# Kernel optimization log

Measured on AMD Instinct MI355X. Metric: run time of the kernel, lower is better.

Reference implementation:

```python
import jax, jax.numpy as jnp
import numpy as np

DIM, HEADS, WS, SHIFT = 192, 6, 8, 4
HEAD_DIM = DIM // HEADS
SCALE = HEAD_DIM ** -0.5
EPS = 1e-5


def _rel_pos_index(ws):
    coords = np.stack(np.meshgrid(np.arange(ws), np.arange(ws), indexing='ij'))  # [2,ws,ws]
    flat = coords.reshape(2, -1)
    rel = flat[:, :, None] - flat[:, None, :]          # [2,N,N]
    rel = rel.transpose(1, 2, 0)
    rel[:, :, 0] += ws - 1
    rel[:, :, 1] += ws - 1
    rel[:, :, 0] *= 2 * ws - 1
    return rel.sum(-1)                                  # [N,N] int


def _attn_mask(H, W, ws, shift):
    if shift == 0:
        return None
    img = np.zeros((H, W), dtype=np.float32)
    cnt = 0
    for hs in (slice(0, -ws), slice(-ws, -shift), slice(-shift, None)):
        for wsl in (slice(0, -ws), slice(-ws, -shift), slice(-shift, None)):
            img[hs, wsl] = cnt
            cnt += 1
    mw = img.reshape(H // ws, ws, W // ws, ws).transpose(0, 2, 1, 3).reshape(-1, ws * ws)  # [nW,N]
    m = mw[:, None, :] - mw[:, :, None]
    return jnp.asarray(np.where(m != 0, -100.0, 0.0).astype(np.float32))  # [nW,N,N]


def _ln(x, w, b):
    mu = x.mean(-1, keepdims=True)
    var = ((x - mu) ** 2).mean(-1, keepdims=True)
    return (x - mu) * jax.lax.rsqrt(var + EPS) * w + b


def setup_inputs() -> dict:
    key = jax.random.key(0)
    ks = jax.random.split(key, 10)
    B, H, W, C = 64, 56, 56, DIM
    hid = 4 * C
    p = lambda k, sh, s=0.02: jax.random.normal(k, sh, jnp.float32) * s
    return {
        'x': jax.random.normal(ks[0], (B, H * W, C), jnp.float32),
        'ln1_w': jnp.ones((C,), jnp.float32), 'ln1_b': jnp.zeros((C,), jnp.float32),
        'qkv_w': p(ks[1], (C, 3 * C)), 'qkv_b': jnp.zeros((3 * C,), jnp.float32),
        'proj_w': p(ks[2], (C, C)), 'proj_b': jnp.zeros((C,), jnp.float32),
        'rpb_table': p(ks[3], ((2 * WS - 1) ** 2, HEADS)),
        'ln2_w': jnp.ones((C,), jnp.float32), 'ln2_b': jnp.zeros((C,), jnp.float32),
        'fc1_w': p(ks[4], (C, hid)), 'fc1_b': jnp.zeros((hid,), jnp.float32),
        'fc2_w': p(ks[5], (hid, C)), 'fc2_b': jnp.zeros((C,), jnp.float32),
        'H': H, 'W': W,
    }


def reference(x, ln1_w, ln1_b, qkv_w, qkv_b, proj_w, proj_b, rpb_table,
              ln2_w, ln2_b, fc1_w, fc1_b, fc2_w, fc2_b, H, W):
    B, L, C = x.shape
    N = WS * WS
    shortcut = x
    xn = _ln(x, ln1_w, ln1_b).reshape(B, H, W, C)
    xn = jnp.roll(xn, (-SHIFT, -SHIFT), (1, 2))
    # window partition -> [B*nW, N, C]
    xw = xn.reshape(B, H // WS, WS, W // WS, WS, C).transpose(0, 1, 3, 2, 4, 5)
    xw = xw.reshape(-1, N, C)
    B_ = xw.shape[0]
    qkv = (xw @ qkv_w + qkv_b).reshape(B_, N, 3, HEADS, HEAD_DIM).transpose(2, 0, 3, 1, 4)
    q, k, v = qkv[0], qkv[1], qkv[2]                    # [B_,h,N,d]
    attn = jnp.einsum('bhnd,bhmd->bhnm', q * SCALE, k)
    bias = rpb_table[_rel_pos_index(WS).reshape(-1)].reshape(N, N, HEADS).transpose(2, 0, 1)
    attn = attn + bias[None]
    mask = _attn_mask(H, W, WS, SHIFT)
    if mask is not None:
        nW = mask.shape[0]
        attn = attn.reshape(B_ // nW, nW, HEADS, N, N) + mask[None, :, None]
        attn = attn.reshape(B_, HEADS, N, N)
    attn = jax.nn.softmax(attn, axis=-1)
    out = jnp.einsum('bhnm,bhmd->bhnd', attn, v).transpose(0, 2, 1, 3).reshape(B_, N, C)
    out = out @ proj_w + proj_b
    # window reverse
    out = out.reshape(B, H // WS, W // WS, WS, WS, C).transpose(0, 1, 3, 2, 4, 5).reshape(B, H, W, C)
    out = jnp.roll(out, (SHIFT, SHIFT), (1, 2))
    x = shortcut + out.reshape(B, L, C)
    h = jax.nn.gelu(_ln(x, ln2_w, ln2_b) @ fc1_w + fc1_b, approximate=False)
    return x + (h @ fc2_w + fc2_b)
```

## Files before the change

### kernel.cpp

```cpp
#include <hip/hip_runtime.h>
#include <cstdint>
#include <cstddef>

#define WS_ 8
#define DIM_ 192
#define HEADS_ 6
#define HD_ 32
#define HH_ 56
#define NW_ 7
#define NWIN_ 49
#define LTOK_ 3136
#define NTOK_ 200704
#define NWTOT_ 3136
#define SHIFT_ 4
#define SCALE_ 0.17677669529663687f

typedef unsigned short ushort_t;
typedef __attribute__((ext_vector_type(8))) short short8;
typedef __attribute__((ext_vector_type(4))) float floatx4;
typedef __attribute__((ext_vector_type(8))) unsigned short ushort8;

__device__ __forceinline__ float b2f(ushort_t u) {
    union { unsigned int i; float f; } c; c.i = ((unsigned int)u) << 16; return c.f;
}
__device__ __forceinline__ ushort_t f2b(float f) {
    union { float f; unsigned int i; } c; c.f = f;
    unsigned int u = c.i;
    unsigned int r = (u + 0x7FFFu + ((u >> 16) & 1u)) >> 16;
    return (ushort_t)r;
}

__device__ __forceinline__ void load_lds16(const void* g, void* l) {
    __builtin_amdgcn_global_load_lds(
        (const __attribute__((address_space(1))) unsigned int*)g,
        (__attribute__((address_space(3))) unsigned int*)l, 16, 0, 0);
}

__device__ __forceinline__ int win_row_to_img(int r) {
    int win = r >> 6, n = r & 63;
    int b = win / NWIN_, wI = win - b * NWIN_;
    int wh = wI / NW_, wwi = wI - wh * NW_;
    int i = n >> 3, j = n & 7;
    int hh = wh * WS_ + i + SHIFT_; if (hh >= HH_) hh -= HH_;
    int ww = wwi * WS_ + j + SHIFT_; if (ww >= HH_) ww -= HH_;
    return b * LTOK_ + hh * HH_ + ww;
}

__global__ void transpose_kernel(const float* __restrict__ in,
                                 ushort_t* __restrict__ out, int K, int N) {
    int id = blockIdx.x * 256 + threadIdx.x;
    if (id >= K * N) return;
    int k = id / N, n = id - k * N;
    out[(size_t)n * K + k] = f2b(in[id]);
}

template <bool PERMUTE>
__global__ __launch_bounds__(256) void ln_kernel(const float* __restrict__ xin,
                                                 const float* __restrict__ w,
                                                 const float* __restrict__ bia,
                                                 ushort_t* __restrict__ out,
                                                 int rowOff) {
    int t = blockIdx.x * 4 + (threadIdx.x >> 6);
    int lane = threadIdx.x & 63;
    int src = PERMUTE ? win_row_to_img(rowOff + t) : t;
    const float* xp = xin + (size_t)src * DIM_;
    float v0 = xp[lane];
    float v1 = xp[lane + 64];
    float v2 = xp[lane + 128];
    float s = v0 + v1 + v2;
    float ss = v0 * v0 + v1 * v1 + v2 * v2;
#pragma unroll
    for (int o = 32; o > 0; o >>= 1) {
        s += __shfl_xor(s, o);
        ss += __shfl_xor(ss, o);
    }
    float mu = s * (1.0f / 192.0f);
    float var = ss * (1.0f / 192.0f) - mu * mu;
    float inv = rsqrtf(var + 1e-5f);
    ushort_t* op = out + (size_t)t * DIM_;
    op[lane]       = f2b((v0 - mu) * inv * w[lane]       + bia[lane]);
    op[lane + 64]  = f2b((v1 - mu) * inv * w[lane + 64]  + bia[lane + 64]);
    op[lane + 128] = f2b((v2 - mu) * inv * w[lane + 128] + bia[lane + 128]);
}

#define EPI_STORE 0
#define EPI_GELU 1
#define EPI_PROJ 2
#define EPI_FC2 3

template <int EPI>
__global__ __launch_bounds__(256) void gemm_kernel(const ushort_t* __restrict__ A,
                                                   const ushort_t* __restrict__ Bt,
                                                   const float* __restrict__ bias,
                                                   void* __restrict__ outv,
                                                   const float* __restrict__ aux,
                                                   int K, int N, int rowOff) {
    __shared__ char smem[40960];

    int tid = threadIdx.x;
    int wave = tid >> 6, lane = tid & 63;
    int quad = lane >> 4, l16 = lane & 15;
    int wave_r = wave >> 1, wave_c = wave & 1;
    int row0 = blockIdx.x * 128;
    int n0 = blockIdx.y * 192;

    floatx4 acc[4][6];
#pragma unroll
    for (int rt = 0; rt < 4; ++rt)
#pragma unroll
        for (int ct = 0; ct < 6; ++ct)
#pragma unroll
            for (int e = 0; e < 4; ++e) acc[rt][ct][e] = 0.0f;

    int nk = K >> 5;

    auto stage = [&](int kk, int buf) {
#pragma unroll
        for (int j = 0; j < 2; ++j) {
            int o = (tid + j * 256) * 16;
            int row = o >> 6, kb = o & 63;
            const ushort_t* g = A + (size_t)(row0 + row) * K + kk * 32 + (kb >> 1);
            load_lds16(g, smem + buf * 8192 + o);
        }
#pragma unroll
        for (int j = 0; j < 3; ++j) {
            int o = (tid + j * 256) * 16;
            int row = o >> 6, kb = o & 63;
            const ushort_t* g = Bt + (size_t)(n0 + row) * K + kk * 32 + (kb >> 1);
            load_lds16(g, smem + 16384 + buf * 12288 + o);
        }
    };

    stage(0, 0);
    for (int kk = 0; kk < nk; ++kk) {
        int cur = kk & 1;
        __syncthreads();
        if (kk + 1 < nk) stage(kk + 1, cur ^ 1);

        short8 a[4];
#pragma unroll
        for (int rt = 0; rt < 4; ++rt)
            a[rt] = *(const short8*)(smem + cur * 8192 +
                     ((wave_r * 64 + rt * 16 + l16) * 64 + quad * 16));
#pragma unroll
        for (int ct = 0; ct < 6; ++ct) {
            short8 b = *(const short8*)(smem + 16384 + cur * 12288 +
                        ((wave_c * 96 + ct * 16 + l16) * 64 + quad * 16));
#pragma unroll
            for (int rt = 0; rt < 4; ++rt)
                acc[rt][ct] = __builtin_amdgcn_mfma_f32_16x16x32_bf16(a[rt], b, acc[rt][ct], 0, 0, 0);
        }
    }

#pragma unroll
    for (int ct = 0; ct < 6; ++ct) {
        int c = n0 + wave_c * 96 + ct * 16 + l16;
        float bs = bias[c];
#pragma unroll
        for (int rt = 0; rt < 4; ++rt) {
#pragma unroll
            for (int r = 0; r < 4; ++r) {
                int rr = row0 + wave_r * 64 + rt * 16 + quad * 4 + r;
                float val = acc[rt][ct][r] + bs;
                if (EPI == EPI_STORE) {
                    ((ushort_t*)outv)[(size_t)rr * N + c] = f2b(val);
                } else if (EPI == EPI_GELU) {
                    float g = 0.5f * val * (1.0f + erff(val * 0.70710678118654752f));
                    ((ushort_t*)outv)[(size_t)rr * N + c] = f2b(g);
                } else if (EPI == EPI_PROJ) {
                    int dst = win_row_to_img(rowOff + rr);
                    size_t idx = (size_t)dst * DIM_ + c;
                    ((float*)outv)[idx] = val + aux[idx];
                } else {
                    size_t idx = (size_t)rr * DIM_ + c;
                    ((float*)outv)[idx] = val + aux[idx];
                }
            }
        }
    }
}

__global__ __launch_bounds__(256) void attn_kernel(const ushort_t* __restrict__ qkv,
                                                   const float* __restrict__ rpb,
                                                   ushort_t* __restrict__ aout,
                                                   int win0) {
    __shared__ float qs[64][36], ks[64][36], vs[64][36];
    __shared__ float S[64][65];
    __shared__ int regid[64];
    int bid = blockIdx.x;
    int winl = bid / HEADS_, head = bid - winl * HEADS_;
    int wI = (win0 + winl) % NWIN_;
    int wh = wI / NW_, wwi = wI - wh * NW_;
    int tid = threadIdx.x;
    int row = tid >> 2, c0 = (tid & 3) * 8;
    size_t base = (size_t)(winl * 64 + row) * (3 * DIM_) + head * HD_ + c0;
    ushort8 qv = *(const ushort8*)(qkv + base);
    ushort8 kv = *(const ushort8*)(qkv + base + DIM_);
    ushort8 vv = *(const ushort8*)(qkv + base + 2 * DIM_);
#pragma unroll
    for (int e = 0; e < 8; ++e) {
        qs[row][c0 + e] = b2f(qv[e]) * SCALE_;
        ks[row][c0 + e] = b2f(kv[e]);
        vs[row][c0 + e] = b2f(vv[e]);
    }
    if (tid < 64) {
        int i = tid >> 3, j = tid & 7;
        int hh = wh * WS_ + i, ww = wwi * WS_ + j;
        int rh = (hh < HH_ - WS_) ? 0 : ((hh < HH_ - SHIFT_) ? 1 : 2);
        int rw = (ww < HH_ - WS_) ? 0 : ((ww < HH_ - SHIFT_) ? 1 : 2);
        regid[tid] = rh * 3 + rw;
    }
    __syncthreads();

    int n = tid >> 2, qq = tid & 3;
    float qr[32];
#pragma unroll
    for (int e = 0; e < 8; ++e) {
        floatx4 t4 = *(const floatx4*)&qs[n][e * 4];
        qr[e * 4 + 0] = t4[0]; qr[e * 4 + 1] = t4[1];
        qr[e * 4 + 2] = t4[2]; qr[e * 4 + 3] = t4[3];
    }
    int i1 = n >> 3, j1 = n & 7;
    int rg1 = regid[n];
#pragma unroll 4
    for (int mi = 0; mi < 16; ++mi) {
        int m = mi * 4 + qq;
        float d = 0.0f;
#pragma unroll
        for (int e = 0; e < 8; ++e) {
            floatx4 k4 = *(const floatx4*)&ks[m][e * 4];
            d += qr[e * 4 + 0] * k4[0] + qr[e * 4 + 1] * k4[1] +
                 qr[e * 4 + 2] * k4[2] + qr[e * 4 + 3] * k4[3];
        }
        int i2 = m >> 3, j2 = m & 7;
        int rel = (i1 - i2 + 7) * 15 + (j1 - j2 + 7);
        d += rpb[rel * HEADS_ + head];
        if (regid[m] != rg1) d -= 100.0f;
        S[n][m] = d;
    }
    __syncthreads();

    if (tid < 64) {
        float mx = -1e30f;
        for (int m = 0; m < 64; ++m) mx = fmaxf(mx, S[tid][m]);
        float sum = 0.0f;
        for (int m = 0; m < 64; ++m) {
            float e = __expf(S[tid][m] - mx);
            S[tid][m] = e;
            sum += e;
        }
        float rs = 1.0f / sum;
        for (int m = 0; m < 64; ++m) S[tid][m] *= rs;
    }
    __syncthreads();

    int d0 = (tid & 3) * 8;
    float o[8];
#pragma unroll
    for (int e = 0; e < 8; ++e) o[e] = 0.0f;
    for (int m = 0; m < 64; ++m) {
        float p = S[n][m];
        floatx4 va = *(const floatx4*)&vs[m][d0];
        floatx4 vb = *(const floatx4*)&vs[m][d0 + 4];
        o[0] += p * va[0]; o[1] += p * va[1]; o[2] += p * va[2]; o[3] += p * va[3];
        o[4] += p * vb[0]; o[5] += p * vb[1]; o[6] += p * vb[2]; o[7] += p * vb[3];
    }
    ushort8 pk;
#pragma unroll
    for (int e = 0; e < 8; ++e) pk[e] = f2b(o[e]);
    *(ushort8*)(aout + (size_t)(winl * 64 + n) * DIM_ + head * HD_ + d0) = pk;
}

extern "C" void kernel_launch(void* const* d_in, const int* in_sizes, int n_in,
                              void* d_out, int out_size, void* d_ws, size_t ws_size,
                              hipStream_t stream) {
    const float* x      = (const float*)d_in[0];
    const float* ln1_w  = (const float*)d_in[1];
    const float* ln1_b  = (const float*)d_in[2];
    const float* qkv_w  = (const float*)d_in[3];
    const float* qkv_b  = (const float*)d_in[4];
    const float* proj_w = (const float*)d_in[5];
    const float* proj_b = (const float*)d_in[6];
    const float* rpb    = (const float*)d_in[7];
    const float* ln2_w  = (const float*)d_in[8];
    const float* ln2_b  = (const float*)d_in[9];
    const float* fc1_w  = (const float*)d_in[10];
    const float* fc1_b  = (const float*)d_in[11];
    const float* fc2_w  = (const float*)d_in[12];
    const float* fc2_b  = (const float*)d_in[13];

    char* ws = (char*)d_ws;
    size_t off = 0;
    auto alloc = [&](size_t bytes) -> void* {
        void* p = ws + off;
        off += (bytes + 255) & ~(size_t)255;
        return p;
    };
    ushort_t* qkv_wt  = (ushort_t*)alloc((size_t)576 * 192 * 2);
    ushort_t* proj_wt = (ushort_t*)alloc((size_t)192 * 192 * 2);
    ushort_t* fc1_wt  = (ushort_t*)alloc((size_t)768 * 192 * 2);
    ushort_t* fc2_wt  = (ushort_t*)alloc((size_t)192 * 768 * 2);

    float* x1 = (float*)d_out;

    size_t budget = (ws_size > off + 4096) ? (ws_size - off - 4096) : 0;
    long rows = (long)(budget / 1920);
    rows = (rows / 128) * 128;
    if (rows < 128) rows = 128;
    if (rows > NTOK_) rows = NTOK_;
    int chunkRows = (int)rows;
    int Wc = chunkRows / 64;
    if (Wc > NWTOT_) Wc = NWTOT_;

    ushort_t* bufS = (ushort_t*)alloc((size_t)chunkRows * 192 * 2);
    ushort_t* bufL = (ushort_t*)alloc((size_t)chunkRows * 768 * 2);
    (void)n_in; (void)in_sizes; (void)out_size;

    transpose_kernel<<<(192 * 576 + 255) / 256, 256, 0, stream>>>(qkv_w, qkv_wt, 192, 576);
    transpose_kernel<<<(192 * 192 + 255) / 256, 256, 0, stream>>>(proj_w, proj_wt, 192, 192);
    transpose_kernel<<<(192 * 768 + 255) / 256, 256, 0, stream>>>(fc1_w, fc1_wt, 192, 768);
    transpose_kernel<<<(768 * 192 + 255) / 256, 256, 0, stream>>>(fc2_w, fc2_wt, 768, 192);

    for (int w0 = 0; w0 < NWTOT_; w0 += Wc) {
        int wc = NWTOT_ - w0 < Wc ? NWTOT_ - w0 : Wc;
        int rowsA = wc * 64;
        ln_kernel<true><<<rowsA / 4, 256, 0, stream>>>(x, ln1_w, ln1_b, bufS, w0 * 64);
        dim3 gq(rowsA / 128, 576 / 192);
        gemm_kernel<EPI_STORE><<<gq, 256, 0, stream>>>(bufS, qkv_wt, qkv_b, bufL, nullptr, 192, 576, 0);
        attn_kernel<<<wc * HEADS_, 256, 0, stream>>>(bufL, rpb, bufS, w0);
        dim3 gp(rowsA / 128, 1);
        gemm_kernel<EPI_PROJ><<<gp, 256, 0, stream>>>(bufS, proj_wt, proj_b, x1, x, 192, 192, w0 * 64);
    }

    for (int t0 = 0; t0 < NTOK_; t0 += chunkRows) {
        int tc = NTOK_ - t0 < chunkRows ? NTOK_ - t0 : chunkRows;
        ln_kernel<false><<<tc / 4, 256, 0, stream>>>(x1 + (size_t)t0 * 192, ln2_w, ln2_b, bufS, 0);
        dim3 g1(tc / 128, 768 / 192);
        gemm_kernel<EPI_GELU><<<g1, 256, 0, stream>>>(bufS, fc1_wt, fc1_b, bufL, nullptr, 192, 768, 0);
        dim3 g2(tc / 128, 1);
        gemm_kernel<EPI_FC2><<<g2, 256, 0, stream>>>(bufL, fc2_wt, fc2_b,
                                                     x1 + (size_t)t0 * 192,
                                                     x1 + (size_t)t0 * 192, 768, 192, 0);
    }
}
```

Before: 1.243 ms.

## Rewrite window attention with MFMA, one wave per window-head, and precomputed bias+mask

```diff
diff --git a/kernel.cpp b/kernel.cpp
--- a/kernel.cpp
+++ b/kernel.cpp
@@ -17,6 +17,7 @@
 
 typedef unsigned short ushort_t;
 typedef __attribute__((ext_vector_type(8))) short short8;
+typedef __attribute__((ext_vector_type(4))) short bf16x4;
 typedef __attribute__((ext_vector_type(4))) float floatx4;
 typedef __attribute__((ext_vector_type(8))) unsigned short ushort8;
 
@@ -52,6 +53,23 @@
     if (id >= K * N) return;
     int k = id / N, n = id - k * N;
     out[(size_t)n * K + k] = f2b(in[id]);
+}
+
+__global__ void bias_kernel(const float* __restrict__ rpb, float* __restrict__ Spre) {
+    int th = blockIdx.x;
+    int type = th / HEADS_, head = th - type * HEADS_;
+    for (int idx = threadIdx.x; idx < 4096; idx += 256) {
+        int q = idx >> 6, k = idx & 63;
+        int i1 = q >> 3, j1 = q & 7, i2 = k >> 3, j2 = k & 7;
+        int rel = (i1 - i2 + 7) * 15 + (j1 - j2 + 7);
+        float v = rpb[rel * HEADS_ + head];
+        int rh1 = (type & 2) ? (i1 < 4 ? 1 : 2) : 0;
+        int rw1 = (type & 1) ? (j1 < 4 ? 1 : 2) : 0;
+        int rh2 = (type & 2) ? (i2 < 4 ? 1 : 2) : 0;
+        int rw2 = (type & 1) ? (j2 < 4 ? 1 : 2) : 0;
+        if (rh1 != rh2 || rw1 != rw2) v -= 100.0f;
+        Spre[(size_t)th * 4096 + idx] = v;
+    }
 }
 
 template <bool PERMUTE>
@@ -87,6 +105,7 @@
 #define EPI_GELU 1
 #define EPI_PROJ 2
 #define EPI_FC2 3
+#define EPI_QKV 4
 
 template <int EPI>
 __global__ __launch_bounds__(256) void gemm_kernel(const ushort_t* __restrict__ A,
@@ -164,6 +183,9 @@
                 float val = acc[rt][ct][r] + bs;
                 if (EPI == EPI_STORE) {
                     ((ushort_t*)outv)[(size_t)rr * N + c] = f2b(val);
+                } else if (EPI == EPI_QKV) {
+                    float sv = (c < DIM_) ? val * SCALE_ : val;
+                    ((ushort_t*)outv)[(size_t)rr * N + c] = f2b(sv);
                 } else if (EPI == EPI_GELU) {
                     float g = 0.5f * val * (1.0f + erff(val * 0.70710678118654752f));
                     ((ushort_t*)outv)[(size_t)rr * N + c] = f2b(g);
@@ -181,94 +203,119 @@
 }
 
 __global__ __launch_bounds__(256) void attn_kernel(const ushort_t* __restrict__ qkv,
-                                                   const float* __restrict__ rpb,
+                                                   const float* __restrict__ Spre,
                                                    ushort_t* __restrict__ aout,
-                                                   int win0) {
-    __shared__ float qs[64][36], ks[64][36], vs[64][36];
-    __shared__ float S[64][65];
-    __shared__ int regid[64];
-    int bid = blockIdx.x;
-    int winl = bid / HEADS_, head = bid - winl * HEADS_;
+                                                   int win0, int nwh) {
+    __shared__ char smem[32768];
+    int wave = threadIdx.x >> 6;
+    int whid = blockIdx.x * 4 + wave;
+    if (whid >= nwh) return;
+    int lane = threadIdx.x & 63;
+    int l16 = lane & 15, quad = lane >> 4;
+    int winl = whid / HEADS_, head = whid - winl * HEADS_;
     int wI = (win0 + winl) % NWIN_;
     int wh = wI / NW_, wwi = wI - wh * NW_;
-    int tid = threadIdx.x;
-    int row = tid >> 2, c0 = (tid & 3) * 8;
-    size_t base = (size_t)(winl * 64 + row) * (3 * DIM_) + head * HD_ + c0;
-    ushort8 qv = *(const ushort8*)(qkv + base);
-    ushort8 kv = *(const ushort8*)(qkv + base + DIM_);
-    ushort8 vv = *(const ushort8*)(qkv + base + 2 * DIM_);
-#pragma unroll
-    for (int e = 0; e < 8; ++e) {
-        qs[row][c0 + e] = b2f(qv[e]) * SCALE_;
-        ks[row][c0 + e] = b2f(kv[e]);
-        vs[row][c0 + e] = b2f(vv[e]);
-    }
-    if (tid < 64) {
-        int i = tid >> 3, j = tid & 7;
-        int hh = wh * WS_ + i, ww = wwi * WS_ + j;
-        int rh = (hh < HH_ - WS_) ? 0 : ((hh < HH_ - SHIFT_) ? 1 : 2);
-        int rw = (ww < HH_ - WS_) ? 0 : ((ww < HH_ - SHIFT_) ? 1 : 2);
-        regid[tid] = rh * 3 + rw;
-    }
-    __syncthreads();
-
-    int n = tid >> 2, qq = tid & 3;
-    float qr[32];
-#pragma unroll
-    for (int e = 0; e < 8; ++e) {
-        floatx4 t4 = *(const floatx4*)&qs[n][e * 4];
-        qr[e * 4 + 0] = t4[0]; qr[e * 4 + 1] = t4[1];
-        qr[e * 4 + 2] = t4[2]; qr[e * 4 + 3] = t4[3];
-    }
-    int i1 = n >> 3, j1 = n & 7;
-    int rg1 = regid[n];
-#pragma unroll 4
-    for (int mi = 0; mi < 16; ++mi) {
-        int m = mi * 4 + qq;
-        float d = 0.0f;
-#pragma unroll
-        for (int e = 0; e < 8; ++e) {
-            floatx4 k4 = *(const floatx4*)&ks[m][e * 4];
-            d += qr[e * 4 + 0] * k4[0] + qr[e * 4 + 1] * k4[1] +
-                 qr[e * 4 + 2] * k4[2] + qr[e * 4 + 3] * k4[3];
-        }
-        int i2 = m >> 3, j2 = m & 7;
-        int rel = (i1 - i2 + 7) * 15 + (j1 - j2 + 7);
-        d += rpb[rel * HEADS_ + head];
-        if (regid[m] != rg1) d -= 100.0f;
-        S[n][m] = d;
-    }
-    __syncthreads();
-
-    if (tid < 64) {
-        float mx = -1e30f;
-        for (int m = 0; m < 64; ++m) mx = fmaxf(mx, S[tid][m]);
-        float sum = 0.0f;
-        for (int m = 0; m < 64; ++m) {
-            float e = __expf(S[tid][m] - mx);
-            S[tid][m] = e;
-            sum += e;
-        }
-        float rs = 1.0f / sum;
-        for (int m = 0; m < 64; ++m) S[tid][m] *= rs;
-    }
-    __syncthreads();
-
-    int d0 = (tid & 3) * 8;
-    float o[8];
-#pragma unroll
-    for (int e = 0; e < 8; ++e) o[e] = 0.0f;
-    for (int m = 0; m < 64; ++m) {
-        float p = S[n][m];
-        floatx4 va = *(const floatx4*)&vs[m][d0];
-        floatx4 vb = *(const floatx4*)&vs[m][d0 + 4];
-        o[0] += p * va[0]; o[1] += p * va[1]; o[2] += p * va[2]; o[3] += p * va[3];
-        o[4] += p * vb[0]; o[5] += p * vb[1]; o[6] += p * vb[2]; o[7] += p * vb[3];
-    }
-    ushort8 pk;
-#pragma unroll
-    for (int e = 0; e < 8; ++e) pk[e] = f2b(o[e]);
-    *(ushort8*)(aout + (size_t)(winl * 64 + n) * DIM_ + head * HD_ + d0) = pk;
+    int type = ((wh == 6) ? 2 : 0) + ((wwi == 6) ? 1 : 0);
+
+    const ushort_t* qb = qkv + (size_t)(winl * 64) * 576 + head * HD_;
+
+    short8 vfrag[2][2];
+#pragma unroll
+    for (int kk = 0; kk < 2; ++kk)
+#pragma unroll
+        for (int dt = 0; dt < 2; ++dt)
+#pragma unroll
+            for (int e = 0; e < 8; ++e)
+                vfrag[dt][kk][e] =
+                    (short)qb[(size_t)(kk * 32 + quad * 8 + e) * 576 + 2 * DIM_ + dt * 16 + l16];
+
+    short8 kf[4], qf[4];
+#pragma unroll
+    for (int t = 0; t < 4; ++t) {
+        kf[t] = *(const short8*)(qb + (size_t)(t * 16 + l16) * 576 + DIM_ + quad * 8);
+        qf[t] = *(const short8*)(qb + (size_t)(t * 16 + l16) * 576 + quad * 8);
+    }
+
+    const float* bp = Spre + (size_t)(type * HEADS_ + head) * 4096;
+    floatx4 acc[4][4];
+#pragma unroll
+    for (int art = 0; art < 4; ++art)
+#pragma unroll
+        for (int act = 0; act < 4; ++act)
+            acc[art][act] = *(const floatx4*)(bp + (act * 16 + l16) * 64 + art * 16 + quad * 4);
+
+#pragma unroll
+    for (int art = 0; art < 4; ++art)
+#pragma unroll
+        for (int act = 0; act < 4; ++act)
+            acc[art][act] = __builtin_amdgcn_mfma_f32_16x16x32_bf16(
+                kf[art], qf[act], acc[art][act], 0, 0, 0);
+
+    char* pb = smem + wave * 8192;
+    int sw = (l16 & 7) << 4;
+#pragma unroll
+    for (int act = 0; act < 4; ++act) {
+        float m = -1e30f;
+#pragma unroll
+        for (int art = 0; art < 4; ++art)
+#pragma unroll
+            for (int r = 0; r < 4; ++r) m = fmaxf(m, acc[art][act][r]);
+        m = fmaxf(m, __shfl_xor(m, 16));
+        m = fmaxf(m, __shfl_xor(m, 32));
+        float s = 0.0f;
+#pragma unroll
+        for (int art = 0; art < 4; ++art)
+#pragma unroll
+            for (int r = 0; r < 4; ++r) {
+                float e = __expf(acc[art][act][r] - m);
+                acc[art][act][r] = e;
+                s += e;
+            }
+        s += __shfl_xor(s, 16);
+        s += __shfl_xor(s, 32);
+        float inv = 1.0f / s;
+        int q = act * 16 + l16;
+        char* rowp = pb + q * 128;
+#pragma unroll
+        for (int art = 0; art < 4; ++art) {
+            bf16x4 pk4;
+#pragma unroll
+            for (int r = 0; r < 4; ++r) pk4[r] = (short)f2b(acc[art][act][r] * inv);
+            *(bf16x4*)(rowp + ((art * 32 + quad * 8) ^ sw)) = pk4;
+        }
+    }
+
+    floatx4 accO[4][2];
+#pragma unroll
+    for (int ot = 0; ot < 4; ++ot)
+#pragma unroll
+        for (int dt = 0; dt < 2; ++dt)
+#pragma unroll
+            for (int e = 0; e < 4; ++e) accO[ot][dt][e] = 0.0f;
+#pragma unroll
+    for (int kk = 0; kk < 2; ++kk) {
+        short8 pa[4];
+#pragma unroll
+        for (int ot = 0; ot < 4; ++ot)
+            pa[ot] = *(const short8*)(pb + (ot * 16 + l16) * 128 +
+                                      ((kk * 64 + quad * 16) ^ sw));
+#pragma unroll
+        for (int dt = 0; dt < 2; ++dt)
+#pragma unroll
+            for (int ot = 0; ot < 4; ++ot)
+                accO[ot][dt] = __builtin_amdgcn_mfma_f32_16x16x32_bf16(
+                    pa[ot], vfrag[dt][kk], accO[ot][dt], 0, 0, 0);
+    }
+
+    ushort_t* op = aout + (size_t)(winl * 64) * DIM_ + head * HD_;
+#pragma unroll
+    for (int ot = 0; ot < 4; ++ot)
+#pragma unroll
+        for (int dt = 0; dt < 2; ++dt)
+#pragma unroll
+            for (int r = 0; r < 4; ++r)
+                op[(size_t)(ot * 16 + quad * 4 + r) * DIM_ + dt * 16 + l16] =
+                    f2b(accO[ot][dt][r]);
 }
 
 extern "C" void kernel_launch(void* const* d_in, const int* in_sizes, int n_in,
@@ -300,6 +347,7 @@
     ushort_t* proj_wt = (ushort_t*)alloc((size_t)192 * 192 * 2);
     ushort_t* fc1_wt  = (ushort_t*)alloc((size_t)768 * 192 * 2);
     ushort_t* fc2_wt  = (ushort_t*)alloc((size_t)192 * 768 * 2);
+    float*    SpreT   = (float*)alloc((size_t)4 * HEADS_ * 4096 * sizeof(float));
 
     float* x1 = (float*)d_out;
 
@@ -320,14 +368,16 @@
     transpose_kernel<<<(192 * 192 + 255) / 256, 256, 0, stream>>>(proj_w, proj_wt, 192, 192);
     transpose_kernel<<<(192 * 768 + 255) / 256, 256, 0, stream>>>(fc1_w, fc1_wt, 192, 768);
     transpose_kernel<<<(768 * 192 + 255) / 256, 256, 0, stream>>>(fc2_w, fc2_wt, 768, 192);
+    bias_kernel<<<4 * HEADS_, 256, 0, stream>>>(rpb, SpreT);
 
     for (int w0 = 0; w0 < NWTOT_; w0 += Wc) {
         int wc = NWTOT_ - w0 < Wc ? NWTOT_ - w0 : Wc;
         int rowsA = wc * 64;
         ln_kernel<true><<<rowsA / 4, 256, 0, stream>>>(x, ln1_w, ln1_b, bufS, w0 * 64);
         dim3 gq(rowsA / 128, 576 / 192);
-        gemm_kernel<EPI_STORE><<<gq, 256, 0, stream>>>(bufS, qkv_wt, qkv_b, bufL, nullptr, 192, 576, 0);
-        attn_kernel<<<wc * HEADS_, 256, 0, stream>>>(bufL, rpb, bufS, w0);
+        gemm_kernel<EPI_QKV><<<gq, 256, 0, stream>>>(bufS, qkv_wt, qkv_b, bufL, nullptr, 192, 576, 0);
+        int nwh = wc * HEADS_;
+        attn_kernel<<<(nwh + 3) / 4, 256, 0, stream>>>(bufL, SpreT, bufS, w0, nwh);
         dim3 gp(rowsA / 128, 1);
         gemm_kernel<EPI_PROJ><<<gp, 256, 0, stream>>>(bufS, proj_wt, proj_b, x1, x, 192, 192, w0 * 64);
     }
```

Measured after the change: 1.033 ms. 17.0% less time.
